# Performance work log

Measured on AMD Instinct MI355X. Metric: run time of the kernel, lower is better.

Reference implementation:

```python
import jax, jax.numpy as jnp
import numpy as np

H = 256  # hidden size

def _lstm_layer(x, W_ih, W_hh, b_ih, b_hh):
    """x: [B, T, I] -> outputs [B, T, H]. PyTorch gate order: i, f, g, o."""
    B, T, _ = x.shape
    # Precompute input projections for all timesteps at once: [B, T, 4H]
    xg = jnp.einsum('bti,gi->btg', x, W_ih) + (b_ih + b_hh)
    xg = jnp.transpose(xg, (1, 0, 2))  # [T, B, 4H]

    def step(carry, xg_t):
        h, c = carry
        gates = xg_t + h @ W_hh.T  # [B, 4H]
        i = jax.nn.sigmoid(gates[:, 0 * H:1 * H])
        f = jax.nn.sigmoid(gates[:, 1 * H:2 * H])
        g = jnp.tanh(gates[:, 2 * H:3 * H])
        o = jax.nn.sigmoid(gates[:, 3 * H:4 * H])
        c = f * c + i * g
        h = o * jnp.tanh(c)
        return (h, c), h

    h0 = jnp.zeros((B, H), dtype=x.dtype)
    c0 = jnp.zeros((B, H), dtype=x.dtype)
    _, ys = jax.lax.scan(step, (h0, c0), xg)  # ys: [T, B, H]
    return jnp.transpose(ys, (1, 0, 2))


def setup_inputs() -> dict:
    key = jax.random.key(0)
    ks = jax.random.split(key, 9)
    B, T, I = 256, 512, 32
    s_in = 1.0 / np.sqrt(H)
    return {
        'M': jax.random.normal(ks[0], (B, T, I), dtype=jnp.float32),
        'W_ih0': jax.random.normal(ks[1], (4 * H, I), dtype=jnp.float32) * s_in,
        'W_hh0': jax.random.normal(ks[2], (4 * H, H), dtype=jnp.float32) * s_in,
        'b_ih0': jax.random.normal(ks[3], (4 * H,), dtype=jnp.float32) * s_in,
        'b_hh0': jax.random.normal(ks[4], (4 * H,), dtype=jnp.float32) * s_in,
        'W_ih1': jax.random.normal(ks[5], (4 * H, H), dtype=jnp.float32) * s_in,
        'W_hh1': jax.random.normal(ks[6], (4 * H, H), dtype=jnp.float32) * s_in,
        'b_ih1': jax.random.normal(ks[7], (4 * H,), dtype=jnp.float32) * s_in,
        'b_hh1': jax.random.normal(ks[8], (4 * H,), dtype=jnp.float32) * s_in,
    }


def reference(M, W_ih0, W_hh0, b_ih0, b_hh0, W_ih1, W_hh1, b_ih1, b_hh1):
    # observations_preprocessor = Identity
    x = _lstm_layer(M, W_ih0, W_hh0, b_ih0, b_hh0)
    x = _lstm_layer(x, W_ih1, W_hh1, b_ih1, b_hh1)
    # hn = rnn_out[:, -1, :]
    return x[:, -1, :]
```

## Files before the change

kernel.cpp:

```cpp
#include <hip/hip_runtime.h>
#include <hip/hip_fp16.h>


#define TT 512
#define HH 256
#define GS 294912

typedef _Float16 f16x8 __attribute__((ext_vector_type(8)));
typedef float    f32x4 __attribute__((ext_vector_type(4)));
typedef unsigned u32x4 __attribute__((ext_vector_type(4)));

__device__ __forceinline__ f16x8 cvt8(const float* p) {
  const float4 a = *(const float4*)p;
  const float4 b = *(const float4*)(p + 4);
  f16x8 r;
  r[0]=(_Float16)a.x; r[1]=(_Float16)a.y; r[2]=(_Float16)a.z; r[3]=(_Float16)a.w;
  r[4]=(_Float16)b.x; r[5]=(_Float16)b.y; r[6]=(_Float16)b.z; r[7]=(_Float16)b.w;
  return r;
}
__device__ __forceinline__ float sigm(float x){ return 1.f/(1.f + __expf(-x)); }
__device__ __forceinline__ float tanh_(float x){ return 1.f - 2.f/(1.f + __expf(2.f*x)); }

__device__ __forceinline__ u32x4 ld16(const void* p) {
  u32x4 r;
  asm volatile("global_load_dwordx4 %0, %1, off sc0 sc1"
               : "=v"(r) : "v"(p) : "memory");
  return r;
}
__device__ __forceinline__ void st2(void* p, unsigned v) {
  asm volatile("global_store_short %0, %1, off sc0 sc1"
               :: "v"(p), "v"(v) : "memory");
}
__device__ __forceinline__ void stp(void* p, unsigned v) {
  asm volatile("global_store_dword %0, %1, off sc0 sc1"
               :: "v"(p), "v"(v) : "memory");
}
__device__ __forceinline__ unsigned ldp(const void* p) {
  unsigned r;
  asm volatile("global_load_dword %0, %1, off sc0 sc1\n\ts_waitcnt vmcnt(0)"
               : "=v"(r) : "v"(p) : "memory");
  return r;
}
__device__ __forceinline__ void wvm0() {
  asm volatile("s_waitcnt vmcnt(0)" ::: "memory");
  __builtin_amdgcn_sched_barrier(0);
}
__device__ __forceinline__ void barrier_lds() {
  __builtin_amdgcn_sched_barrier(0);
  asm volatile("s_waitcnt lgkmcnt(0)" ::: "memory");
  __builtin_amdgcn_s_barrier();
  __builtin_amdgcn_sched_barrier(0);
}

__global__ void init_ws(uint4* p, int n) {
  int i = blockIdx.x * blockDim.x + threadIdx.x;
  if (i >= n) return;
  int rem = i % (GS / 16);
  p[i] = (rem < 17408) ? make_uint4(0x00010001u,0x00010001u,0x00010001u,0x00010001u)
                       : make_uint4(0u,0u,0u,0u);
}

__global__ __launch_bounds__(512) void lstm_v11(
    const float* __restrict__ M,
    const float* __restrict__ Wih0, const float* __restrict__ Whh0,
    const float* __restrict__ bih0, const float* __restrict__ bhh0,
    const float* __restrict__ Wih1, const float* __restrict__ Whh1,
    const float* __restrict__ bih1, const float* __restrict__ bhh1,
    float* __restrict__ out, char* __restrict__ ws)
{
  __shared__ __align__(16) char ldsH[16384];
  __shared__ __align__(16) char ldsX[32768];

  const int tid  = threadIdx.x, lane = tid & 63, wv = tid >> 6;
  const int bid  = blockIdx.x;
  const int g    = bid / 6;
  const int r6   = bid - g * 6;
  const int role = r6 >> 1;
  const int half = r6 & 1;
  const int col16 = lane & 15, ko8 = (lane >> 4) << 3, brow = (lane >> 4) << 2;
  const int unit = half * 128 + wv * 16 + col16;

  char* base   = ws + (size_t)g * GS;
  char* stream = base;
  char* h1r    = base + 131072;
  char* xg     = base + 147456;
  int*  prog   = (int*)(base + 278528);

  const unsigned ubase = ((unsigned)(unit >> 5) << 10)
                       | ((unsigned)((unit >> 3) & 3) << 8)
                       | ((unsigned)(unit & 7) << 1);
  const unsigned pb = (unsigned)(half ^ 1) * 4096;

  f16x8 W[4][8], WI[4];
  float bias[4] = {0.f, 0.f, 0.f, 0.f};
  {
    const float* Wsrc = (role == 0) ? Whh0 : (role == 1) ? Wih1 : Whh1;
    #pragma unroll
    for (int q = 0; q < 4; ++q) {
      const int row = q * HH + unit;
      #pragma unroll
      for (int kt = 0; kt < 8; ++kt)
        W[q][kt] = cvt8(Wsrc + (size_t)row * HH + kt * 32 + ko8);
      if (role == 0) { WI[q] = cvt8(Wih0 + (size_t)row * 32 + ko8);
                       bias[q] = bih0[row] + bhh0[row]; }
      else if (role == 1) bias[q] = bih1[row] + bhh1[row];
    }
  }

  float cst[4] = {0.f, 0.f, 0.f, 0.f};

  if (role == 0) {
    const float* mp = M + (size_t)(g * 16 + col16) * TT * 32 + ko8;
    float4 m0 = *(const float4*)mp, m1 = *(const float4*)(mp + 4);
    int lastW = 0;
    for (int t = 0; t < TT; ++t) {
      const int rpar = (t - 1) & 1;
      if (t >= 1 && tid < 256) {
        const char* a = stream + (size_t)((t - 1) & 15) * 8192 + pb + tid * 16;
        const unsigned pat = (((unsigned)(t - 1) >> 4) & 1u) * 0x00010001u;
        u32x4 v = ld16(a);
        wvm0();
        for (;;) {
          const u32x4 d = (v ^ pat) & 0x00010001u;
          if (__all((d[0] | d[1] | d[2] | d[3]) == 0)) break;
          v = ld16(a);
          wvm0();
        }
        *(u32x4*)(ldsH + rpar * 8192 + pb + tid * 16) = v;
      }
      barrier_lds();
      if (t >= 16) {
        while (lastW < t - 15) {
          const int a = (int)ldp(prog + 0), b = (int)ldp(prog + 1);
          lastW = a < b ? a : b;
        }
      }
      f32x4 acc[4];
      f16x8 am;
      am[0]=(_Float16)m0.x; am[1]=(_Float16)m0.y; am[2]=(_Float16)m0.z; am[3]=(_Float16)m0.w;
      am[4]=(_Float16)m1.x; am[5]=(_Float16)m1.y; am[6]=(_Float16)m1.z; am[7]=(_Float16)m1.w;
      #pragma unroll
      for (int q = 0; q < 4; ++q) {
        acc[q] = (f32x4){bias[q], bias[q], bias[q], bias[q]};
        acc[q] = __builtin_amdgcn_mfma_f32_16x16x32_f16(am, WI[q], acc[q], 0, 0, 0);
      }
      if (t >= 1) {
        #pragma unroll
        for (int kt = 0; kt < 8; ++kt) {
          const f16x8 A = *(const f16x8*)(ldsH + rpar * 8192 + kt * 1024 + lane * 16);
          #pragma unroll
          for (int q = 0; q < 4; ++q)
            acc[q] = __builtin_amdgcn_mfma_f32_16x16x32_f16(A, W[q][kt], acc[q], 0, 0, 0);
        }
      }
      if (t + 1 < TT) { m0 = *(const float4*)(mp + (t + 1) * 32);
                        m1 = *(const float4*)(mp + (t + 1) * 32 + 4); }
      char* slot = stream + (size_t)(t & 15) * 8192;
      const unsigned wt = ((unsigned)t >> 4) & 1u;
      #pragma unroll
      for (int r = 0; r < 4; ++r) {
        const float iv = sigm(acc[0][r]), fv = sigm(acc[1][r]);
        const float gv = tanh_(acc[2][r]), ov = sigm(acc[3][r]);
        cst[r] = fv * cst[r] + iv * gv;
        const float h = ov * tanh_(cst[r]);
        unsigned short hb = __builtin_bit_cast(unsigned short, (_Float16)h);
        hb = (unsigned short)((hb & 0xFFFEu) | wt);
        const unsigned fo = ubase + ((unsigned)(brow + r) << 4);
        st2(slot + fo, (unsigned)hb);
        *(unsigned short*)(ldsH + (t & 1) * 8192 + fo) = hb;
      }
    }
  } else if (role == 1) {
    int lastL = 0;
    for (int t = 0; t < TT; ++t) {
      const char* a = stream + (size_t)(t & 15) * 8192 + tid * 16;
      const unsigned pat = (((unsigned)t >> 4) & 1u) * 0x00010001u;
      u32x4 v = ld16(a);
      wvm0();
      for (;;) {
        const u32x4 d = (v ^ pat) & 0x00010001u;
        if (__all((d[0] | d[1] | d[2] | d[3]) == 0)) break;
        v = ld16(a);
        wvm0();
      }
      *(u32x4*)(ldsX + (t & 1) * 8192 + tid * 16) = v;
      barrier_lds();
      if (tid == 0) stp(prog + half, (unsigned)(t + 1));
      if (t >= 4) { while (lastL < t - 3) lastL = (int)ldp(prog + 2 + half); }
      f32x4 acc[4];
      #pragma unroll
      for (int q = 0; q < 4; ++q)
        acc[q] = (f32x4){bias[q], bias[q], bias[q], bias[q]};
      #pragma unroll
      for (int kt = 0; kt < 8; ++kt) {
        const f16x8 A = *(const f16x8*)(ldsX + (t & 1) * 8192 + kt * 1024 + lane * 16);
        #pragma unroll
        for (int q = 0; q < 4; ++q)
          acc[q] = __builtin_amdgcn_mfma_f32_16x16x32_f16(A, W[q][kt], acc[q], 0, 0, 0);
      }
      char* xs = xg + (size_t)(t & 3) * 32768 + half * 16384;
      const unsigned wtx = ((unsigned)t >> 2) & 1u;
      #pragma unroll
      for (int q = 0; q < 4; ++q)
        #pragma unroll
        for (int r = 0; r < 4; ++r) {
          unsigned short hb = __builtin_bit_cast(unsigned short, (_Float16)acc[q][r]);
          hb = (unsigned short)((hb & 0xFFFEu) | wtx);
          const unsigned off = (unsigned)(brow + r) * 1024
                             + (unsigned)(q * 128 + wv * 16 + col16) * 2;
          st2(xs + off, (unsigned)hb);
        }
    }
  } else {
    for (int t = 0; t < TT; ++t) {
      const int rpar = (t - 1) & 1;
      const char* sx = xg + (size_t)(t & 3) * 32768 + half * 16384;
      const unsigned patX = (((unsigned)t >> 2) & 1u) * 0x00010001u;
      const char* sa = h1r + (size_t)rpar * 8192 + pb + tid * 16;
      const unsigned patA = (((unsigned)(t - 1) >> 1) & 1u) * 0x00010001u;
      const bool hasA = (t >= 1) && (tid < 256);
      u32x4 x0 = ld16(sx + tid * 32), x1 = ld16(sx + tid * 32 + 16), va;
      if (hasA) va = ld16(sa);
      wvm0();
      for (;;) {
        u32x4 d = ((x0 ^ patX) | (x1 ^ patX)) & 0x00010001u;
        unsigned bad = d[0] | d[1] | d[2] | d[3];
        if (hasA) { const u32x4 e = (va ^ patA) & 0x00010001u;
                    bad |= e[0] | e[1] | e[2] | e[3]; }
        if (__all(bad == 0)) break;
        x0 = ld16(sx + tid * 32); x1 = ld16(sx + tid * 32 + 16);
        if (hasA) va = ld16(sa);
        wvm0();
      }
      *(u32x4*)(ldsX + (t & 1) * 16384 + tid * 32)      = x0;
      *(u32x4*)(ldsX + (t & 1) * 16384 + tid * 32 + 16) = x1;
      if (hasA) *(u32x4*)(ldsH + rpar * 8192 + pb + tid * 16) = va;
      barrier_lds();
      if (tid == 0) stp(prog + 2 + half, (unsigned)(t + 1));
      f32x4 acc[4];
      #pragma unroll
      for (int q = 0; q < 4; ++q) acc[q] = (f32x4){0.f, 0.f, 0.f, 0.f};
      if (t >= 1) {
        #pragma unroll
        for (int kt = 0; kt < 8; ++kt) {
          const f16x8 A = *(const f16x8*)(ldsH + rpar * 8192 + kt * 1024 + lane * 16);
          #pragma unroll
          for (int q = 0; q < 4; ++q)
            acc[q] = __builtin_amdgcn_mfma_f32_16x16x32_f16(A, W[q][kt], acc[q], 0, 0, 0);
        }
      }
      const char* xl = ldsX + (t & 1) * 16384;
      #pragma unroll
      for (int q = 0; q < 4; ++q)
        #pragma unroll
        for (int r = 0; r < 4; ++r) {
          const unsigned short xv = *(const unsigned short*)
            (xl + (brow + r) * 1024 + (q * 128 + wv * 16 + col16) * 2);
          acc[q][r] += (float)__builtin_bit_cast(_Float16, xv);
        }
      char* d1 = h1r + (size_t)(t & 1) * 8192;
      const unsigned wt = ((unsigned)t >> 1) & 1u;
      #pragma unroll
      for (int r = 0; r < 4; ++r) {
        const float iv = sigm(acc[0][r]), fv = sigm(acc[1][r]);
        const float gv = tanh_(acc[2][r]), ov = sigm(acc[3][r]);
        cst[r] = fv * cst[r] + iv * gv;
        const float h = ov * tanh_(cst[r]);
        if (t < TT - 1) {
          unsigned short hb = __builtin_bit_cast(unsigned short, (_Float16)h);
          hb = (unsigned short)((hb & 0xFFFEu) | wt);
          const unsigned fo = ubase + ((unsigned)(brow + r) << 4);
          st2(d1 + fo, (unsigned)hb);
          *(unsigned short*)(ldsH + (t & 1) * 8192 + fo) = hb;
        } else {
          out[(size_t)(g * 16 + brow + r) * HH + unit] = h;
        }
      }
    }
  }
}

__global__ void fb_init(uint4* p, int n) {
  int i = blockIdx.x * blockDim.x + threadIdx.x;
  if (i < n) p[i] = make_uint4(0x00010001u,0x00010001u,0x00010001u,0x00010001u);
}
__device__ __forceinline__ unsigned fb_tg(int t){ return ((unsigned)(t + 4) >> 1) & 1u; }

__global__ __launch_bounds__(512) void lstm_v9(
    const float* __restrict__ M,
    const float* __restrict__ Wih0, const float* __restrict__ Whh0,
    const float* __restrict__ bih0, const float* __restrict__ bhh0,
    const float* __restrict__ Wih1, const float* __restrict__ Whh1,
    const float* __restrict__ bih1, const float* __restrict__ bhh1,
    float* __restrict__ out, char* __restrict__ ws)
{
  __shared__ __align__(16) char  ldsA[16384];
  __shared__ __align__(16) f32x4 xch[8][64];
  const int tid  = threadIdx.x, lane = tid & 63, wv = tid >> 6;
  const int g = blockIdx.x & 7, w = blockIdx.x >> 3;
  const int hf = wv & 1, role = wv >> 1;
  const int col16 = lane & 15, ko8 = (lane >> 4) << 3;
  const int unit = w * 16 + col16;
  #define H0R(slot) (ws + (((g << 1) | (slot)) << 14))
  #define H1R(slot) (ws + 262144 + (((g << 1) | (slot)) << 14))
  f16x8 W0[4][8], WI[4];
  float bias[4] = {0.f, 0.f, 0.f, 0.f};
  if (role == 0) {
    #pragma unroll
    for (int q = 0; q < 4; ++q) {
      const int row = q * HH + unit;
      #pragma unroll
      for (int kt = 0; kt < 8; ++kt) W0[q][kt] = cvt8(Whh0 + (size_t)row*HH + kt*32 + ko8);
      WI[q] = cvt8(Wih0 + (size_t)row*32 + ko8); bias[q] = bih0[row] + bhh0[row];
    }
  } else if (role == 1) {
    #pragma unroll
    for (int q = 0; q < 4; ++q) {
      const int row = q * HH + unit;
      #pragma unroll
      for (int kt = 0; kt < 8; ++kt) W0[q][kt] = cvt8(Wih1 + (size_t)row*HH + kt*32 + ko8);
      bias[q] = bih1[row] + bhh1[row];
    }
  } else if (role == 2) {
    #pragma unroll
    for (int q = 0; q < 4; ++q) {
      const int row = q * HH + unit;
      #pragma unroll
      for (int kt = 0; kt < 8; ++kt) W0[q][kt] = cvt8(Whh1 + (size_t)row*HH + kt*32 + ko8);
    }
  }
  const int sl = tid & 63, skt = (tid >> 6) & 7;
  const unsigned moff0 = (unsigned)((sl & 15) * 512 + skt * 64 + (sl >> 4) * 16);
  const unsigned moff1 = moff0 + 16 * 512;
  const unsigned lo    = (unsigned)(skt * 1024 + sl * 16);
  const unsigned hoff = (((unsigned)(hf*16 + col16)) << 9) | ((unsigned)(lane >> 4) << 4);
  unsigned soff[4];
  #pragma unroll
  for (int r = 0; r < 4; ++r)
    soff[r] = (((unsigned)(hf*16 + ((lane>>4)<<2) + r)) << 9) | ((unsigned)unit << 1);
  const float* mp = M + (size_t)(g*32 + hf*16 + col16) * TT * 32 + ko8;
  float4 m0 = {0,0,0,0}, m1 = {0,0,0,0};
  if (role == 0) { m0 = *(const float4*)mp; m1 = *(const float4*)(mp + 4); }
  float cst[4] = {0.f, 0.f, 0.f, 0.f};
  for (int p = 0; p <= TT; ++p) {
    if (p >= 1) {
      const char* s = H0R((p - 1) & 1);
      const unsigned pat = fb_tg(p - 1) * 0x00010001u;
      u32x4 v0 = ld16(s + moff0), v1 = ld16(s + moff1);
      wvm0();
      for (;;) {
        const u32x4 d = ((v0 ^ pat) | (v1 ^ pat)) & 0x00010001u;
        if (__all((d[0] | d[1] | d[2] | d[3]) == 0)) break;
        v0 = ld16(s + moff0); v1 = ld16(s + moff1); wvm0();
      }
      *(u32x4*)(ldsA + lo) = v0; *(u32x4*)(ldsA + 8192 + lo) = v1;
    }
    barrier_lds();
    f32x4 acc[4];
    if (role == 0 && p < TT) {
      f16x8 am;
      am[0]=(_Float16)m0.x; am[1]=(_Float16)m0.y; am[2]=(_Float16)m0.z; am[3]=(_Float16)m0.w;
      am[4]=(_Float16)m1.x; am[5]=(_Float16)m1.y; am[6]=(_Float16)m1.z; am[7]=(_Float16)m1.w;
      #pragma unroll
      for (int q = 0; q < 4; ++q) {
        acc[q] = (f32x4){bias[q], bias[q], bias[q], bias[q]};
        acc[q] = __builtin_amdgcn_mfma_f32_16x16x32_f16(am, WI[q], acc[q], 0, 0, 0);
      }
      if (p >= 1) {
        #pragma unroll
        for (int kt = 0; kt < 8; ++kt) {
          const f16x8 A = *(const f16x8*)(ldsA + hf*8192 + kt*1024 + lane*16);
          #pragma unroll
          for (int q = 0; q < 4; ++q)
            acc[q] = __builtin_amdgcn_mfma_f32_16x16x32_f16(A, W0[q][kt], acc[q], 0, 0, 0);
        }
      }
      char* d = H0R(p & 1);
      const unsigned wt = fb_tg(p);
      #pragma unroll
      for (int r = 0; r < 4; ++r) {
        const float iv = sigm(acc[0][r]), fv = sigm(acc[1][r]);
        const float gv = tanh_(acc[2][r]), ov = sigm(acc[3][r]);
        cst[r] = fv * cst[r] + iv * gv;
        const float h = ov * tanh_(cst[r]);
        unsigned short hb = __builtin_bit_cast(unsigned short, (_Float16)h);
        hb = (unsigned short)((hb & 0xFFFEu) | wt);
        st2(d + soff[r], (unsigned)hb);
      }
      if (p + 1 < TT) { m0 = *(const float4*)(mp + (p+1)*32); m1 = *(const float4*)(mp + (p+1)*32 + 4); }
    } else if (role == 1 && p >= 1) {
      #pragma unroll
      for (int q = 0; q < 4; ++q) acc[q] = (f32x4){bias[q], bias[q], bias[q], bias[q]};
      #pragma unroll
      for (int kt = 0; kt < 8; ++kt) {
        const f16x8 A = *(const f16x8*)(ldsA + hf*8192 + kt*1024 + lane*16);
        #pragma unroll
        for (int q = 0; q < 4; ++q)
          acc[q] = __builtin_amdgcn_mfma_f32_16x16x32_f16(A, W0[q][kt], acc[q], 0, 0, 0);
      }
    } else if (role == 2 && p >= 2) {
      const char* s = H1R(p & 1);
      const unsigned pat = fb_tg(p - 2) * 0x00010001u;
      u32x4 hb[8];
      #pragma unroll
      for (int k = 0; k < 8; ++k) hb[k] = ld16(s + hoff + k*64);
      wvm0();
      for (;;) {
        unsigned bad = 0;
        #pragma unroll
        for (int k = 0; k < 8; ++k) {
          const u32x4 d = (hb[k] ^ pat) & 0x00010001u;
          bad |= d[0] | d[1] | d[2] | d[3];
        }
        if (__all(bad == 0)) break;
        #pragma unroll
        for (int k = 0; k < 8; ++k) hb[k] = ld16(s + hoff + k*64);
        wvm0();
      }
      #pragma unroll
      for (int q = 0; q < 4; ++q) acc[q] = (f32x4){0.f, 0.f, 0.f, 0.f};
      #pragma unroll
      for (int kt = 0; kt < 8; ++kt) {
        const f16x8 A = __builtin_bit_cast(f16x8, hb[kt]);
        #pragma unroll
        for (int q = 0; q < 4; ++q)
          acc[q] = __builtin_amdgcn_mfma_f32_16x16x32_f16(A, W0[q][kt], acc[q], 0, 0, 0);
      }
      #pragma unroll
      for (int q = 0; q < 4; ++q) xch[hf*4 + q][lane] = acc[q];
    }
    barrier_lds();
    if (role == 1 && p >= 1) {
      if (p >= 2) {
        #pragma unroll
        for (int q = 0; q < 4; ++q) acc[q] = acc[q] + xch[hf*4 + q][lane];
      }
      if (p < TT) {
        char* d = H1R((p - 1) & 1);
        const unsigned wt = fb_tg(p - 1);
        #pragma unroll
        for (int r = 0; r < 4; ++r) {
          const float iv = sigm(acc[0][r]), fv = sigm(acc[1][r]);
          const float gv = tanh_(acc[2][r]), ov = sigm(acc[3][r]);
          cst[r] = fv * cst[r] + iv * gv;
          const float h = ov * tanh_(cst[r]);
          unsigned short hb = __builtin_bit_cast(unsigned short, (_Float16)h);
          hb = (unsigned short)((hb & 0xFFFEu) | wt);
          st2(d + soff[r], (unsigned)hb);
        }
      } else {
        #pragma unroll
        for (int r = 0; r < 4; ++r) {
          const float iv = sigm(acc[0][r]), fv = sigm(acc[1][r]);
          const float gv = tanh_(acc[2][r]), ov = sigm(acc[3][r]);
          cst[r] = fv * cst[r] + iv * gv;
          const float h = ov * tanh_(cst[r]);
          const int b = hf*16 + ((lane>>4)<<2) + r;
          out[(size_t)(g*32 + b) * HH + (w*16 + col16)] = h;
        }
      }
    }
  }
  #undef H0R
  #undef H1R
}

extern "C" void kernel_launch(void* const* d_in, const int* in_sizes, int n_in,
                              void* d_out, int out_size, void* d_ws, size_t ws_size,
                              hipStream_t stream) {
  (void)in_sizes; (void)n_in; (void)out_size;
  const float* M    = (const float*)d_in[0];
  const float* Wih0 = (const float*)d_in[1];
  const float* Whh0 = (const float*)d_in[2];
  const float* bih0 = (const float*)d_in[3];
  const float* bhh0 = (const float*)d_in[4];
  const float* Wih1 = (const float*)d_in[5];
  const float* Whh1 = (const float*)d_in[6];
  const float* bih1 = (const float*)d_in[7];
  const float* bhh1 = (const float*)d_in[8];

  if (ws_size >= (size_t)16 * GS) {
    const int n16 = 16 * (GS / 16);
    init_ws<<<(n16 + 255) / 256, 256, 0, stream>>>((uint4*)d_ws, n16);
    lstm_v11<<<96, 512, 0, stream>>>(M, Wih0, Whh0, bih0, bhh0,
                                     Wih1, Whh1, bih1, bhh1,
                                     (float*)d_out, (char*)d_ws);
  } else {
    if (ws_size < 524288) return;
    fb_init<<<128, 256, 0, stream>>>((uint4*)d_ws, 32768);
    lstm_v9<<<128, 512, 0, stream>>>(M, Wih0, Whh0, bih0, bhh0,
                                     Wih1, Whh1, bih1, bhh1,
                                     (float*)d_out, (char*)d_ws);
  }
}
```

Before: 1.486 ms.

## Overlap peer hidden-state fetch with local-half MFMAs, feed registers directly

Each wave now loads the peer block's half of the previous hidden state straight from global memory into registers, instead of having 256 threads spin-wait and stage it through LDS before the barrier. The local half of the K dimension is computed from LDS first, while the remote loads are in flight. The flag-validated spin-wait happens only afterwards, and the remote half's MFMAs read the registers directly. The aim is to hide cross-block latency behind compute and drop an LDS store. The cost is that every wave now issues the same redundant global loads and polls on its own.

New measurement: 4.862 ms. +227.2%, slower.

```diff
diff --git a/kernel.cpp b/kernel.cpp
--- a/kernel.cpp
+++ b/kernel.cpp
@@ -60,7 +60,7 @@
                        : make_uint4(0u,0u,0u,0u);
 }
 
-__global__ __launch_bounds__(512) void lstm_v11(
+__global__ __launch_bounds__(512) void lstm_v14(
     const float* __restrict__ M,
     const float* __restrict__ Wih0, const float* __restrict__ Whh0,
     const float* __restrict__ bih0, const float* __restrict__ bhh0,
@@ -90,6 +90,8 @@
                        | ((unsigned)((unit >> 3) & 3) << 8)
                        | ((unsigned)(unit & 7) << 1);
   const unsigned pb = (unsigned)(half ^ 1) * 4096;
+  const int lk = half * 4;
+  const int pk = (half ^ 1) * 4;
 
   f16x8 W[4][8], WI[4];
   float bias[4] = {0.f, 0.f, 0.f, 0.f};
@@ -115,18 +117,11 @@
     int lastW = 0;
     for (int t = 0; t < TT; ++t) {
       const int rpar = (t - 1) & 1;
-      if (t >= 1 && tid < 256) {
-        const char* a = stream + (size_t)((t - 1) & 15) * 8192 + pb + tid * 16;
-        const unsigned pat = (((unsigned)(t - 1) >> 4) & 1u) * 0x00010001u;
-        u32x4 v = ld16(a);
-        wvm0();
-        for (;;) {
-          const u32x4 d = (v ^ pat) & 0x00010001u;
-          if (__all((d[0] | d[1] | d[2] | d[3]) == 0)) break;
-          v = ld16(a);
-          wvm0();
-        }
-        *(u32x4*)(ldsH + rpar * 8192 + pb + tid * 16) = v;
+      u32x4 pf[4];
+      if (t >= 1) {
+        const char* a = stream + (size_t)((t - 1) & 15) * 8192 + pb + lane * 16;
+        #pragma unroll
+        for (int i = 0; i < 4; ++i) pf[i] = ld16(a + i * 1024);
       }
       barrier_lds();
       if (t >= 16) {
@@ -146,11 +141,33 @@
       }
       if (t >= 1) {
         #pragma unroll
-        for (int kt = 0; kt < 8; ++kt) {
-          const f16x8 A = *(const f16x8*)(ldsH + rpar * 8192 + kt * 1024 + lane * 16);
+        for (int i = 0; i < 4; ++i) {
+          const f16x8 A = *(const f16x8*)(ldsH + rpar * 8192 + (lk + i) * 1024 + lane * 16);
           #pragma unroll
           for (int q = 0; q < 4; ++q)
-            acc[q] = __builtin_amdgcn_mfma_f32_16x16x32_f16(A, W[q][kt], acc[q], 0, 0, 0);
+            acc[q] = __builtin_amdgcn_mfma_f32_16x16x32_f16(A, W[q][lk + i], acc[q], 0, 0, 0);
+        }
+        const unsigned pat = (((unsigned)(t - 1) >> 4) & 1u) * 0x00010001u;
+        const char* a = stream + (size_t)((t - 1) & 15) * 8192 + pb + lane * 16;
+        wvm0();
+        for (;;) {
+          unsigned bad = 0;
+          #pragma unroll
+          for (int i = 0; i < 4; ++i) {
+            const u32x4 d = (pf[i] ^ pat) & 0x00010001u;
+            bad |= d[0] | d[1] | d[2] | d[3];
+          }
+          if (__all(bad == 0)) break;
+          #pragma unroll
+          for (int i = 0; i < 4; ++i) pf[i] = ld16(a + i * 1024);
+          wvm0();
+        }
+        #pragma unroll
+        for (int i = 0; i < 4; ++i) {
+          const f16x8 A = __builtin_bit_cast(f16x8, pf[i]);
+          #pragma unroll
+          for (int q = 0; q < 4; ++q)
+            acc[q] = __builtin_amdgcn_mfma_f32_16x16x32_f16(A, W[q][pk + i], acc[q], 0, 0, 0);
         }
       }
       if (t + 1 < TT) { m0 = *(const float4*)(mp + (t + 1) * 32);
@@ -214,27 +231,24 @@
   } else {
     for (int t = 0; t < TT; ++t) {
       const int rpar = (t - 1) & 1;
+      u32x4 pf[4];
+      const char* pa = h1r + (size_t)rpar * 8192 + pb + lane * 16;
+      if (t >= 1) {
+        #pragma unroll
+        for (int i = 0; i < 4; ++i) pf[i] = ld16(pa + i * 1024);
+      }
       const char* sx = xg + (size_t)(t & 3) * 32768 + half * 16384;
       const unsigned patX = (((unsigned)t >> 2) & 1u) * 0x00010001u;
-      const char* sa = h1r + (size_t)rpar * 8192 + pb + tid * 16;
-      const unsigned patA = (((unsigned)(t - 1) >> 1) & 1u) * 0x00010001u;
-      const bool hasA = (t >= 1) && (tid < 256);
-      u32x4 x0 = ld16(sx + tid * 32), x1 = ld16(sx + tid * 32 + 16), va;
-      if (hasA) va = ld16(sa);
+      u32x4 x0 = ld16(sx + tid * 32), x1 = ld16(sx + tid * 32 + 16);
       wvm0();
       for (;;) {
-        u32x4 d = ((x0 ^ patX) | (x1 ^ patX)) & 0x00010001u;
-        unsigned bad = d[0] | d[1] | d[2] | d[3];
-        if (hasA) { const u32x4 e = (va ^ patA) & 0x00010001u;
-                    bad |= e[0] | e[1] | e[2] | e[3]; }
-        if (__all(bad == 0)) break;
+        const u32x4 d = ((x0 ^ patX) | (x1 ^ patX)) & 0x00010001u;
+        if (__all((d[0] | d[1] | d[2] | d[3]) == 0)) break;
         x0 = ld16(sx + tid * 32); x1 = ld16(sx + tid * 32 + 16);
-        if (hasA) va = ld16(sa);
         wvm0();
       }
       *(u32x4*)(ldsX + (t & 1) * 16384 + tid * 32)      = x0;
       *(u32x4*)(ldsX + (t & 1) * 16384 + tid * 32 + 16) = x1;
-      if (hasA) *(u32x4*)(ldsH + rpar * 8192 + pb + tid * 16) = va;
       barrier_lds();
       if (tid == 0) stp(prog + 2 + half, (unsigned)(t + 1));
       f32x4 acc[4];
@@ -242,11 +256,31 @@
       for (int q = 0; q < 4; ++q) acc[q] = (f32x4){0.f, 0.f, 0.f, 0.f};
       if (t >= 1) {
         #pragma unroll
-        for (int kt = 0; kt < 8; ++kt) {
-          const f16x8 A = *(const f16x8*)(ldsH + rpar * 8192 + kt * 1024 + lane * 16);
+        for (int i = 0; i < 4; ++i) {
+          const f16x8 A = *(const f16x8*)(ldsH + rpar * 8192 + (lk + i) * 1024 + lane * 16);
           #pragma unroll
           for (int q = 0; q < 4; ++q)
-            acc[q] = __builtin_amdgcn_mfma_f32_16x16x32_f16(A, W[q][kt], acc[q], 0, 0, 0);
+            acc[q] = __builtin_amdgcn_mfma_f32_16x16x32_f16(A, W[q][lk + i], acc[q], 0, 0, 0);
+        }
+        const unsigned patA = (((unsigned)(t - 1) >> 1) & 1u) * 0x00010001u;
+        for (;;) {
+          unsigned bad = 0;
+          #pragma unroll
+          for (int i = 0; i < 4; ++i) {
+            const u32x4 d = (pf[i] ^ patA) & 0x00010001u;
+            bad |= d[0] | d[1] | d[2] | d[3];
+          }
+          if (__all(bad == 0)) break;
+          #pragma unroll
+          for (int i = 0; i < 4; ++i) pf[i] = ld16(pa + i * 1024);
+          wvm0();
+        }
+        #pragma unroll
+        for (int i = 0; i < 4; ++i) {
+          const f16x8 A = __builtin_bit_cast(f16x8, pf[i]);
+          #pragma unroll
+          for (int q = 0; q < 4; ++q)
+            acc[q] = __builtin_amdgcn_mfma_f32_16x16x32_f16(A, W[q][pk + i], acc[q], 0, 0, 0);
         }
       }
       const char* xl = ldsX + (t & 1) * 16384;
@@ -482,7 +516,7 @@
   if (ws_size >= (size_t)16 * GS) {
     const int n16 = 16 * (GS / 16);
     init_ws<<<(n16 + 255) / 256, 256, 0, stream>>>((uint4*)d_ws, n16);
-    lstm_v11<<<96, 512, 0, stream>>>(M, Wih0, Whh0, bih0, bhh0,
+    lstm_v14<<<96, 512, 0, stream>>>(M, Wih0, Whh0, bih0, bhh0,
                                      Wih1, Whh1, bih1, bhh1,
                                      (float*)d_out, (char*)d_ws);
   } else {
```

## Split each LSTM role across four 256-thread blocks per batch group

Applied to the files above, without the earlier changes.

Each role (layer-0 recurrence, layer-1 input projection, layer-1 recurrence) is now split across four 256-thread workgroups instead of two 512-thread ones, giving 192 blocks so more CUs run the recurrence with fewer waves per block. Every block now reads the full hidden state back from global memory each step rather than merging its own half through LDS. The progress-flag wait in layer 0 is moved after the MMA work and reads four counters with one vector load. The per-step cross-block sync and the global flag polling now involve more blocks, which may raise latency on the serial critical path.

Result: faster. 1.199 ms (-19.4%).

```diff
diff --git a/kernel.cpp b/kernel.cpp
--- a/kernel.cpp
+++ b/kernel.cpp
@@ -41,6 +41,12 @@
                : "=v"(r) : "v"(p) : "memory");
   return r;
 }
+__device__ __forceinline__ u32x4 ldp4(const void* p) {
+  u32x4 r;
+  asm volatile("global_load_dwordx4 %0, %1, off sc0 sc1\n\ts_waitcnt vmcnt(0)"
+               : "=v"(r) : "v"(p) : "memory");
+  return r;
+}
 __device__ __forceinline__ void wvm0() {
   asm volatile("s_waitcnt vmcnt(0)" ::: "memory");
   __builtin_amdgcn_sched_barrier(0);
@@ -60,7 +66,7 @@
                        : make_uint4(0u,0u,0u,0u);
 }
 
-__global__ __launch_bounds__(512) void lstm_v11(
+__global__ __launch_bounds__(256, 1) void lstm_v16(
     const float* __restrict__ M,
     const float* __restrict__ Wih0, const float* __restrict__ Whh0,
     const float* __restrict__ bih0, const float* __restrict__ bhh0,
@@ -68,17 +74,17 @@
     const float* __restrict__ bih1, const float* __restrict__ bhh1,
     float* __restrict__ out, char* __restrict__ ws)
 {
-  __shared__ __align__(16) char ldsH[16384];
-  __shared__ __align__(16) char ldsX[32768];
+  __shared__ __align__(16) char ldsA[16384];
+  __shared__ __align__(16) char ldsB[16384];
 
   const int tid  = threadIdx.x, lane = tid & 63, wv = tid >> 6;
   const int bid  = blockIdx.x;
-  const int g    = bid / 6;
-  const int r6   = bid - g * 6;
-  const int role = r6 >> 1;
-  const int half = r6 & 1;
+  const int g    = bid / 12;
+  const int idx  = bid - g * 12;
+  const int role = idx >> 2;
+  const int q4   = idx & 3;
   const int col16 = lane & 15, ko8 = (lane >> 4) << 3, brow = (lane >> 4) << 2;
-  const int unit = half * 128 + wv * 16 + col16;
+  const int unit = q4 * 64 + wv * 16 + col16;
 
   char* base   = ws + (size_t)g * GS;
   char* stream = base;
@@ -89,7 +95,6 @@
   const unsigned ubase = ((unsigned)(unit >> 5) << 10)
                        | ((unsigned)((unit >> 3) & 3) << 8)
                        | ((unsigned)(unit & 7) << 1);
-  const unsigned pb = (unsigned)(half ^ 1) * 4096;
 
   f16x8 W[4][8], WI[4];
   float bias[4] = {0.f, 0.f, 0.f, 0.f};
@@ -114,27 +119,22 @@
     float4 m0 = *(const float4*)mp, m1 = *(const float4*)(mp + 4);
     int lastW = 0;
     for (int t = 0; t < TT; ++t) {
-      const int rpar = (t - 1) & 1;
-      if (t >= 1 && tid < 256) {
-        const char* a = stream + (size_t)((t - 1) & 15) * 8192 + pb + tid * 16;
+      const int par = t & 1;
+      if (t >= 1) {
+        const char* s = stream + (size_t)((t - 1) & 15) * 8192 + tid * 16;
         const unsigned pat = (((unsigned)(t - 1) >> 4) & 1u) * 0x00010001u;
-        u32x4 v = ld16(a);
+        u32x4 v0 = ld16(s), v1 = ld16(s + 4096);
         wvm0();
         for (;;) {
-          const u32x4 d = (v ^ pat) & 0x00010001u;
+          const u32x4 d = ((v0 ^ pat) | (v1 ^ pat)) & 0x00010001u;
           if (__all((d[0] | d[1] | d[2] | d[3]) == 0)) break;
-          v = ld16(a);
+          v0 = ld16(s); v1 = ld16(s + 4096);
           wvm0();
         }
-        *(u32x4*)(ldsH + rpar * 8192 + pb + tid * 16) = v;
+        *(u32x4*)(ldsA + par * 8192 + tid * 16)        = v0;
+        *(u32x4*)(ldsA + par * 8192 + tid * 16 + 4096) = v1;
       }
       barrier_lds();
-      if (t >= 16) {
-        while (lastW < t - 15) {
-          const int a = (int)ldp(prog + 0), b = (int)ldp(prog + 1);
-          lastW = a < b ? a : b;
-        }
-      }
       f32x4 acc[4];
       f16x8 am;
       am[0]=(_Float16)m0.x; am[1]=(_Float16)m0.y; am[2]=(_Float16)m0.z; am[3]=(_Float16)m0.w;
@@ -147,7 +147,7 @@
       if (t >= 1) {
         #pragma unroll
         for (int kt = 0; kt < 8; ++kt) {
-          const f16x8 A = *(const f16x8*)(ldsH + rpar * 8192 + kt * 1024 + lane * 16);
+          const f16x8 A = *(const f16x8*)(ldsA + par * 8192 + kt * 1024 + lane * 16);
           #pragma unroll
           for (int q = 0; q < 4; ++q)
             acc[q] = __builtin_amdgcn_mfma_f32_16x16x32_f16(A, W[q][kt], acc[q], 0, 0, 0);
@@ -155,6 +155,16 @@
       }
       if (t + 1 < TT) { m0 = *(const float4*)(mp + (t + 1) * 32);
                         m1 = *(const float4*)(mp + (t + 1) * 32 + 4); }
+      if (t >= 16) {
+        while (lastW < t - 15) {
+          const u32x4 d = ldp4(prog);
+          int m = (int)d[0];
+          m = m < (int)d[1] ? m : (int)d[1];
+          m = m < (int)d[2] ? m : (int)d[2];
+          m = m < (int)d[3] ? m : (int)d[3];
+          lastW = m;
+        }
+      }
       char* slot = stream + (size_t)(t & 15) * 8192;
       const unsigned wt = ((unsigned)t >> 4) & 1u;
       #pragma unroll
@@ -165,40 +175,42 @@
         const float h = ov * tanh_(cst[r]);
         unsigned short hb = __builtin_bit_cast(unsigned short, (_Float16)h);
         hb = (unsigned short)((hb & 0xFFFEu) | wt);
-        const unsigned fo = ubase + ((unsigned)(brow + r) << 4);
-        st2(slot + fo, (unsigned)hb);
-        *(unsigned short*)(ldsH + (t & 1) * 8192 + fo) = hb;
+        st2(slot + ubase + ((unsigned)(brow + r) << 4), (unsigned)hb);
       }
     }
   } else if (role == 1) {
     int lastL = 0;
     for (int t = 0; t < TT; ++t) {
-      const char* a = stream + (size_t)(t & 15) * 8192 + tid * 16;
-      const unsigned pat = (((unsigned)t >> 4) & 1u) * 0x00010001u;
-      u32x4 v = ld16(a);
-      wvm0();
-      for (;;) {
-        const u32x4 d = (v ^ pat) & 0x00010001u;
-        if (__all((d[0] | d[1] | d[2] | d[3]) == 0)) break;
-        v = ld16(a);
+      const int par = t & 1;
+      {
+        const char* s = stream + (size_t)(t & 15) * 8192 + tid * 16;
+        const unsigned pat = (((unsigned)t >> 4) & 1u) * 0x00010001u;
+        u32x4 v0 = ld16(s), v1 = ld16(s + 4096);
         wvm0();
-      }
-      *(u32x4*)(ldsX + (t & 1) * 8192 + tid * 16) = v;
+        for (;;) {
+          const u32x4 d = ((v0 ^ pat) | (v1 ^ pat)) & 0x00010001u;
+          if (__all((d[0] | d[1] | d[2] | d[3]) == 0)) break;
+          v0 = ld16(s); v1 = ld16(s + 4096);
+          wvm0();
+        }
+        *(u32x4*)(ldsA + par * 8192 + tid * 16)        = v0;
+        *(u32x4*)(ldsA + par * 8192 + tid * 16 + 4096) = v1;
+      }
       barrier_lds();
-      if (tid == 0) stp(prog + half, (unsigned)(t + 1));
-      if (t >= 4) { while (lastL < t - 3) lastL = (int)ldp(prog + 2 + half); }
+      if (tid == 0) stp(prog + q4, (unsigned)(t + 1));
+      if (t >= 4) { while (lastL < t - 3) lastL = (int)ldp(prog + 4 + q4); }
       f32x4 acc[4];
       #pragma unroll
       for (int q = 0; q < 4; ++q)
         acc[q] = (f32x4){bias[q], bias[q], bias[q], bias[q]};
       #pragma unroll
       for (int kt = 0; kt < 8; ++kt) {
-        const f16x8 A = *(const f16x8*)(ldsX + (t & 1) * 8192 + kt * 1024 + lane * 16);
+        const f16x8 A = *(const f16x8*)(ldsA + par * 8192 + kt * 1024 + lane * 16);
         #pragma unroll
         for (int q = 0; q < 4; ++q)
           acc[q] = __builtin_amdgcn_mfma_f32_16x16x32_f16(A, W[q][kt], acc[q], 0, 0, 0);
       }
-      char* xs = xg + (size_t)(t & 3) * 32768 + half * 16384;
+      char* xs = xg + (size_t)(t & 3) * 32768 + q4 * 8192;
       const unsigned wtx = ((unsigned)t >> 2) & 1u;
       #pragma unroll
       for (int q = 0; q < 4; ++q)
@@ -206,59 +218,66 @@
         for (int r = 0; r < 4; ++r) {
           unsigned short hb = __builtin_bit_cast(unsigned short, (_Float16)acc[q][r]);
           hb = (unsigned short)((hb & 0xFFFEu) | wtx);
-          const unsigned off = (unsigned)(brow + r) * 1024
-                             + (unsigned)(q * 128 + wv * 16 + col16) * 2;
+          const unsigned off = (unsigned)(brow + r) * 512
+                             + (unsigned)(q * 64 + wv * 16 + col16) * 2;
           st2(xs + off, (unsigned)hb);
         }
     }
   } else {
     for (int t = 0; t < TT; ++t) {
-      const int rpar = (t - 1) & 1;
-      const char* sx = xg + (size_t)(t & 3) * 32768 + half * 16384;
-      const unsigned patX = (((unsigned)t >> 2) & 1u) * 0x00010001u;
-      const char* sa = h1r + (size_t)rpar * 8192 + pb + tid * 16;
-      const unsigned patA = (((unsigned)(t - 1) >> 1) & 1u) * 0x00010001u;
-      const bool hasA = (t >= 1) && (tid < 256);
-      u32x4 x0 = ld16(sx + tid * 32), x1 = ld16(sx + tid * 32 + 16), va;
-      if (hasA) va = ld16(sa);
-      wvm0();
-      for (;;) {
-        u32x4 d = ((x0 ^ patX) | (x1 ^ patX)) & 0x00010001u;
-        unsigned bad = d[0] | d[1] | d[2] | d[3];
-        if (hasA) { const u32x4 e = (va ^ patA) & 0x00010001u;
-                    bad |= e[0] | e[1] | e[2] | e[3]; }
-        if (__all(bad == 0)) break;
-        x0 = ld16(sx + tid * 32); x1 = ld16(sx + tid * 32 + 16);
-        if (hasA) va = ld16(sa);
+      const int par = t & 1;
+      {
+        const char* sx = xg + (size_t)(t & 3) * 32768 + q4 * 8192 + tid * 16;
+        const unsigned patX = (((unsigned)t >> 2) & 1u) * 0x00010001u;
+        const char* sh = h1r + (size_t)((t - 1) & 1) * 8192 + tid * 16;
+        const unsigned patH = (((unsigned)(t - 1) >> 1) & 1u) * 0x00010001u;
+        const bool hasH = (t >= 1);
+        u32x4 x0 = ld16(sx), x1 = ld16(sx + 4096), h0v, h1v;
+        if (hasH) { h0v = ld16(sh); h1v = ld16(sh + 4096); }
         wvm0();
-      }
-      *(u32x4*)(ldsX + (t & 1) * 16384 + tid * 32)      = x0;
-      *(u32x4*)(ldsX + (t & 1) * 16384 + tid * 32 + 16) = x1;
-      if (hasA) *(u32x4*)(ldsH + rpar * 8192 + pb + tid * 16) = va;
+        for (;;) {
+          u32x4 d = ((x0 ^ patX) | (x1 ^ patX)) & 0x00010001u;
+          unsigned bad = d[0] | d[1] | d[2] | d[3];
+          if (hasH) {
+            const u32x4 e = ((h0v ^ patH) | (h1v ^ patH)) & 0x00010001u;
+            bad |= e[0] | e[1] | e[2] | e[3];
+          }
+          if (__all(bad == 0)) break;
+          x0 = ld16(sx); x1 = ld16(sx + 4096);
+          if (hasH) { h0v = ld16(sh); h1v = ld16(sh + 4096); }
+          wvm0();
+        }
+        *(u32x4*)(ldsB + par * 8192 + tid * 16)        = x0;
+        *(u32x4*)(ldsB + par * 8192 + tid * 16 + 4096) = x1;
+        if (hasH) {
+          *(u32x4*)(ldsA + par * 8192 + tid * 16)        = h0v;
+          *(u32x4*)(ldsA + par * 8192 + tid * 16 + 4096) = h1v;
+        }
+      }
       barrier_lds();
-      if (tid == 0) stp(prog + 2 + half, (unsigned)(t + 1));
+      if (tid == 0) stp(prog + 4 + q4, (unsigned)(t + 1));
       f32x4 acc[4];
       #pragma unroll
       for (int q = 0; q < 4; ++q) acc[q] = (f32x4){0.f, 0.f, 0.f, 0.f};
       if (t >= 1) {
         #pragma unroll
         for (int kt = 0; kt < 8; ++kt) {
-          const f16x8 A = *(const f16x8*)(ldsH + rpar * 8192 + kt * 1024 + lane * 16);
+          const f16x8 A = *(const f16x8*)(ldsA + par * 8192 + kt * 1024 + lane * 16);
           #pragma unroll
           for (int q = 0; q < 4; ++q)
             acc[q] = __builtin_amdgcn_mfma_f32_16x16x32_f16(A, W[q][kt], acc[q], 0, 0, 0);
         }
       }
-      const char* xl = ldsX + (t & 1) * 16384;
+      const char* xl = ldsB + par * 8192;
       #pragma unroll
       for (int q = 0; q < 4; ++q)
         #pragma unroll
         for (int r = 0; r < 4; ++r) {
           const unsigned short xv = *(const unsigned short*)
-            (xl + (brow + r) * 1024 + (q * 128 + wv * 16 + col16) * 2);
+            (xl + (brow + r) * 512 + (q * 64 + wv * 16 + col16) * 2);
           acc[q][r] += (float)__builtin_bit_cast(_Float16, xv);
         }
-      char* d1 = h1r + (size_t)(t & 1) * 8192;
+      char* d1 = h1r + (size_t)par * 8192;
       const unsigned wt = ((unsigned)t >> 1) & 1u;
       #pragma unroll
       for (int r = 0; r < 4; ++r) {
@@ -269,9 +288,7 @@
         if (t < TT - 1) {
           unsigned short hb = __builtin_bit_cast(unsigned short, (_Float16)h);
           hb = (unsigned short)((hb & 0xFFFEu) | wt);
-          const unsigned fo = ubase + ((unsigned)(brow + r) << 4);
-          st2(d1 + fo, (unsigned)hb);
-          *(unsigned short*)(ldsH + (t & 1) * 8192 + fo) = hb;
+          st2(d1 + ubase + ((unsigned)(brow + r) << 4), (unsigned)hb);
         } else {
           out[(size_t)(g * 16 + brow + r) * HH + unit] = h;
         }
@@ -482,9 +499,9 @@
   if (ws_size >= (size_t)16 * GS) {
     const int n16 = 16 * (GS / 16);
     init_ws<<<(n16 + 255) / 256, 256, 0, stream>>>((uint4*)d_ws, n16);
-    lstm_v11<<<96, 512, 0, stream>>>(M, Wih0, Whh0, bih0, bhh0,
-                                     Wih1, Whh1, bih1, bhh1,
-                                     (float*)d_out, (char*)d_ws);
+    lstm_v16<<<192, 256, 0, stream>>>(M, Wih0, Whh0, bih0, bhh0,
+                                      Wih1, Whh1, bih1, bhh1,
+                                      (float*)d_out, (char*)d_ws);
   } else {
     if (ws_size < 524288) return;
     fb_init<<<128, 256, 0, stream>>>((uint4*)d_ws, 32768);
```
